# Kernel optimization log

Hardware: AMD Instinct MI355X
Metric: run time of the kernel (lower is better)

## Reference

```python
import jax, jax.numpy as jnp
import numpy as np

N = 100_000      # nodes
E = 1_600_000    # edges (avg degree 16)
D = 64           # input_dim
H = 64           # hidden_dim
G = 2048         # graphs in batch
EPS = 1e-5       # BatchNorm eps


def setup_inputs() -> dict:
    key = jax.random.key(0)
    ks = jax.random.split(key, 12)
    x = jax.random.normal(ks[0], (N, D), dtype=jnp.float32)
    edge_index = jax.random.randint(ks[1], (2, E), 0, N, dtype=jnp.int64)
    batch = jnp.sort(jax.random.randint(ks[2], (N,), 0, G, dtype=jnp.int64))
    s = 1.0 / np.sqrt(D)
    W1 = jax.random.normal(ks[3], (D, H), dtype=jnp.float32) * s
    b1 = jnp.zeros((H,), jnp.float32)
    g1 = jnp.ones((H,), jnp.float32)
    bt1 = jnp.zeros((H,), jnp.float32)
    W2 = jax.random.normal(ks[4], (H, H), dtype=jnp.float32) * s
    b2 = jnp.zeros((H,), jnp.float32)
    g2 = jnp.ones((H,), jnp.float32)
    bt2 = jnp.zeros((H,), jnp.float32)
    return {"x": x, "edge_index": edge_index, "batch": batch,
            "W1": W1, "b1": b1, "g1": g1, "bt1": bt1,
            "W2": W2, "b2": b2, "g2": g2, "bt2": bt2,
            "num_graphs": G}


def reference(x, edge_index, batch, W1, b1, g1, bt1, W2, b2, g2, bt2, num_graphs):
    n = x.shape[0]
    # GCN normalization with added self-loops (PyG GCNConv default)
    loops = jnp.arange(n, dtype=edge_index.dtype)
    src = jnp.concatenate([edge_index[0], loops])
    dst = jnp.concatenate([edge_index[1], loops])
    deg = jax.ops.segment_sum(jnp.ones(src.shape, jnp.float32), dst, num_segments=n)
    dis = jax.lax.rsqrt(jnp.maximum(deg, 1.0))  # deg >= 1 with self-loops
    norm = dis[src] * dis[dst]                  # [E+N]

    def gcn(h, W, b):
        h = h @ W                               # [N,H] dense transform first
        msg = h[src] * norm[:, None]            # gather + scale  [E+N, H]
        return jax.ops.segment_sum(msg, dst, num_segments=n) + b

    def bn(h, gamma, beta):
        mu = h.mean(axis=0)
        var = h.var(axis=0)
        return (h - mu) * jax.lax.rsqrt(var + EPS) * gamma + beta

    h = jax.nn.relu(bn(gcn(x, W1, b1), g1, bt1))
    h = jax.nn.relu(bn(gcn(h, W2, b2), g2, bt2))

    # global mean pool over graph ids
    ones = jnp.ones((n,), jnp.float32)
    counts = jax.ops.segment_sum(ones, batch, num_segments=num_graphs)
    sums = jax.ops.segment_sum(h, batch, num_segments=num_graphs)
    return sums / jnp.maximum(counts, 1.0)[:, None]
```

## Files before the change

kernel.cpp:

```cpp
#include <hip/hip_runtime.h>
#include <hip/hip_bf16.h>

#define BN_EPS 1e-5f
#define CCHUNK 8192

__device__ __forceinline__ float bf2f(ushort u) {
    return __uint_as_float(((unsigned int)u) << 16);
}
__device__ __forceinline__ ushort f2bf(float f) {
    unsigned int u = __float_as_uint(f);
    u += 0x7FFFu + ((u >> 16) & 1u);
    return (ushort)(u >> 16);
}

__global__ void k_bhist(const int* __restrict__ dst, int E, int nb, int* __restrict__ bktcnt) {
    __shared__ int lh[1024];
    for (int j = threadIdx.x; j < nb; j += 256) lh[j] = 0;
    __syncthreads();
    for (int i = blockIdx.x * blockDim.x + threadIdx.x; i < E; i += gridDim.x * blockDim.x)
        atomicAdd(&lh[dst[i] >> 7], 1);
    __syncthreads();
    for (int j = threadIdx.x; j < nb; j += 256) {
        int c = lh[j];
        if (c) atomicAdd(&bktcnt[j], c);
    }
}

__global__ void k_bscan(const int* __restrict__ bktcnt, int nb, int N,
                        int* __restrict__ bktoff, int* __restrict__ gpos,
                        int* __restrict__ rowptr) {
    __shared__ int sh[256];
    int tid = threadIdx.x;
    int base = tid * 4;
    int v[4]; int tsum = 0;
    #pragma unroll
    for (int k = 0; k < 4; ++k) {
        int i = base + k;
        v[k] = (i < nb) ? bktcnt[i] : 0;
        tsum += v[k];
    }
    sh[tid] = tsum;
    __syncthreads();
    for (int off = 1; off < 256; off <<= 1) {
        int add = (tid >= off) ? sh[tid - off] : 0;
        __syncthreads();
        sh[tid] += add;
        __syncthreads();
    }
    int excl = sh[tid] - tsum;
    #pragma unroll
    for (int k = 0; k < 4; ++k) {
        int i = base + k;
        if (i <= nb) {
            bktoff[i] = excl;
            if (i < nb) gpos[i] = excl;
        }
        excl += v[k];
    }
    if (tid == 255) rowptr[N] = sh[255];
}

__global__ void k_partition(const int* __restrict__ src, const int* __restrict__ dst,
                            int E, int nb, int sb,
                            int* __restrict__ gpos, unsigned int* __restrict__ eb) {
    __shared__ int lh[1024];
    int e0 = blockIdx.x * CCHUNK;
    int cnt = min(CCHUNK, E - e0);
    for (int j = threadIdx.x; j < nb; j += 256) lh[j] = 0;
    __syncthreads();
    for (int k = threadIdx.x; k < cnt; k += 256)
        atomicAdd(&lh[dst[e0 + k] >> 7], 1);
    __syncthreads();
    for (int j = threadIdx.x; j < nb; j += 256) {
        int c = lh[j];
        if (c) lh[j] = atomicAdd(&gpos[j], c);
    }
    __syncthreads();
    for (int k = threadIdx.x; k < cnt; k += 256) {
        int d = dst[e0 + k];
        unsigned int s = (unsigned int)src[e0 + k];
        int pos = atomicAdd(&lh[d >> 7], 1);
        eb[pos] = (((unsigned int)(d & 127)) << sb) | s;
    }
}

__global__ void k_row(const unsigned int* __restrict__ eb, const int* __restrict__ bktoff,
                      int sb, int N, float* __restrict__ dis, int* __restrict__ rowptr) {
    __shared__ int h[128];
    __shared__ int p[128];
    int tid = threadIdx.x;
    int b = blockIdx.x;
    if (tid < 128) h[tid] = 0;
    __syncthreads();
    int e0 = bktoff[b], e1 = bktoff[b + 1];
    for (int e = e0 + tid; e < e1; e += 256)
        atomicAdd(&h[(eb[e] >> sb) & 127], 1);
    __syncthreads();
    if (tid < 128) p[tid] = h[tid];
    __syncthreads();
    for (int off = 1; off < 128; off <<= 1) {
        int add = (tid < 128 && tid >= off) ? p[tid - off] : 0;
        __syncthreads();
        if (tid < 128) p[tid] += add;
        __syncthreads();
    }
    if (tid < 128) {
        int d = b * 128 + tid;
        if (d < N) {
            rowptr[d] = e0 + p[tid] - h[tid];
            dis[d] = rsqrtf((float)(h[tid] + 1));
        }
    }
}

__global__ void k_csrfill(const unsigned int* __restrict__ eb, const int* __restrict__ bktoff,
                          const int* __restrict__ rowptr, const float* __restrict__ dis,
                          int sb, unsigned int smask, int N,
                          int* __restrict__ cs, float* __restrict__ wf) {
    __shared__ int nc[128];
    __shared__ float dl[128];
    int tid = threadIdx.x;
    int b = blockIdx.x;
    if (tid < 128) {
        int d = b * 128 + tid;
        nc[tid] = (d < N) ? rowptr[d] : 0;
        dl[tid] = (d < N) ? dis[d] : 1.f;
    }
    __syncthreads();
    int e0 = bktoff[b], e1 = bktoff[b + 1];
    for (int e = e0 + tid; e < e1; e += 256) {
        unsigned int v = eb[e];
        int dloc = (v >> sb) & 127;
        int s = (int)(v & smask);
        int slot = atomicAdd(&nc[dloc], 1);
        cs[slot] = s;
        wf[slot] = dis[s] * dl[dloc];
    }
}

__global__ void k_matmul64t(const float* __restrict__ X, const float* __restrict__ W,
                            const float* __restrict__ bnp, int n, ushort* __restrict__ tb) {
    __shared__ float Xs[64][68];
    __shared__ float Ws[64][64];
    const int tid = threadIdx.x;
    const int rowbase = blockIdx.x * 64;

    {
        const float4* W4 = (const float4*)W;
        float4* Ws4 = (float4*)&Ws[0][0];
        #pragma unroll
        for (int k = 0; k < 4; ++k) Ws4[tid + 256 * k] = W4[tid + 256 * k];
    }
    {
        const int r  = tid >> 2;
        const int c0 = (tid & 3) * 16;
        const int row = rowbase + r;
        #pragma unroll
        for (int j = 0; j < 4; ++j) {
            float4 v;
            if (row < n) v = *(const float4*)&X[(size_t)row * 64 + c0 + 4 * j];
            else v = make_float4(0.f, 0.f, 0.f, 0.f);
            float vv[4] = {v.x, v.y, v.z, v.w};
            #pragma unroll
            for (int i = 0; i < 4; ++i) {
                int c = c0 + 4 * j + i;
                float f = vv[i];
                if (bnp) f = fmaxf(0.f, fmaf(f, bnp[c], bnp[64 + c]));
                Xs[c][r] = f;
            }
        }
    }
    __syncthreads();

    const int r0 = (tid & 15) * 4;
    const int c0 = (tid >> 4) * 4;
    float acc[4][4];
    #pragma unroll
    for (int i = 0; i < 4; ++i)
        #pragma unroll
        for (int j = 0; j < 4; ++j) acc[i][j] = 0.f;

    #pragma unroll 4
    for (int k = 0; k < 64; ++k) {
        float4 xv = *(const float4*)&Xs[k][r0];
        float4 wv = *(const float4*)&Ws[k][c0];
        float xa[4] = {xv.x, xv.y, xv.z, xv.w};
        float wa[4] = {wv.x, wv.y, wv.z, wv.w};
        #pragma unroll
        for (int i = 0; i < 4; ++i)
            #pragma unroll
            for (int j = 0; j < 4; ++j)
                acc[i][j] = fmaf(xa[i], wa[j], acc[i][j]);
    }

    #pragma unroll
    for (int i = 0; i < 4; ++i) {
        int row = rowbase + r0 + i;
        if (row < n) {
            ushort4 o;
            o.x = f2bf(acc[i][0]); o.y = f2bf(acc[i][1]);
            o.z = f2bf(acc[i][2]); o.w = f2bf(acc[i][3]);
            *(ushort4*)&tb[(size_t)row * 64 + c0] = o;
        }
    }
}

__global__ void k_gather(const int* __restrict__ cs, const float* __restrict__ wf,
                         const int* __restrict__ rowptr, const float* __restrict__ dis,
                         const ushort* __restrict__ tb, int n, float* __restrict__ a) {
    int lane = threadIdx.x & 63;
    int wave = threadIdx.x >> 6;
    int row = blockIdx.x * 4 + wave;
    if (row >= n) return;
    const int fl = lane & 7;
    const int o  = lane >> 3;
    int e0 = rowptr[row], e1 = rowptr[row + 1];
    float acc[8];
    #pragma unroll
    for (int i = 0; i < 8; ++i) acc[i] = 0.f;
    for (int base = e0; base < e1; base += 64) {
        int cnt = min(64, e1 - base);
        int   p  = (lane < cnt) ? cs[base + lane] : 0;
        float wv = (lane < cnt) ? wf[base + lane] : 0.f;
        int nq = (cnt + 7) >> 3;
        for (int j = 0; j < nq; ++j) {
            int idx = 8 * j + o;
            int s = __shfl(p, idx);
            float w = __shfl(wv, idx);
            uint4 tv = *(const uint4*)&tb[(size_t)s * 64 + 8 * fl];
            acc[0] = fmaf(__uint_as_float(tv.x << 16),         w, acc[0]);
            acc[1] = fmaf(__uint_as_float(tv.x & 0xffff0000u), w, acc[1]);
            acc[2] = fmaf(__uint_as_float(tv.y << 16),         w, acc[2]);
            acc[3] = fmaf(__uint_as_float(tv.y & 0xffff0000u), w, acc[3]);
            acc[4] = fmaf(__uint_as_float(tv.z << 16),         w, acc[4]);
            acc[5] = fmaf(__uint_as_float(tv.z & 0xffff0000u), w, acc[5]);
            acc[6] = fmaf(__uint_as_float(tv.w << 16),         w, acc[6]);
            acc[7] = fmaf(__uint_as_float(tv.w & 0xffff0000u), w, acc[7]);
        }
    }
    #pragma unroll
    for (int i = 0; i < 8; ++i) {
        acc[i] += __shfl_xor(acc[i], 8);
        acc[i] += __shfl_xor(acc[i], 16);
        acc[i] += __shfl_xor(acc[i], 32);
    }
    if (o == 0) {
        float dr = dis[row];
        float d2 = dr * dr;
        uint4 ts = *(const uint4*)&tb[(size_t)row * 64 + 8 * fl];
        acc[0] = fmaf(__uint_as_float(ts.x << 16),         d2, acc[0]);
        acc[1] = fmaf(__uint_as_float(ts.x & 0xffff0000u), d2, acc[1]);
        acc[2] = fmaf(__uint_as_float(ts.y << 16),         d2, acc[2]);
        acc[3] = fmaf(__uint_as_float(ts.y & 0xffff0000u), d2, acc[3]);
        acc[4] = fmaf(__uint_as_float(ts.z << 16),         d2, acc[4]);
        acc[5] = fmaf(__uint_as_float(ts.z & 0xffff0000u), d2, acc[5]);
        acc[6] = fmaf(__uint_as_float(ts.w << 16),         d2, acc[6]);
        acc[7] = fmaf(__uint_as_float(ts.w & 0xffff0000u), d2, acc[7]);
        float4 o0 = make_float4(acc[0], acc[1], acc[2], acc[3]);
        float4 o1 = make_float4(acc[4], acc[5], acc[6], acc[7]);
        *(float4*)&a[(size_t)row * 64 + 8 * fl]     = o0;
        *(float4*)&a[(size_t)row * 64 + 8 * fl + 4] = o1;
    }
}

__global__ void k_stats(const float* __restrict__ a, int n, float* __restrict__ stats) {
    int c = threadIdx.x & 63;
    int grp = threadIdx.x >> 6;
    float s = 0.f, s2 = 0.f;
    for (int r = blockIdx.x * 4 + grp; r < n; r += gridDim.x * 4) {
        float v = a[(size_t)r * 64 + c];
        s += v; s2 += v * v;
    }
    __shared__ float sh[2][4][64];
    sh[0][grp][c] = s; sh[1][grp][c] = s2;
    __syncthreads();
    if (threadIdx.x < 64) {
        float S  = sh[0][0][c] + sh[0][1][c] + sh[0][2][c] + sh[0][3][c];
        float S2 = sh[1][0][c] + sh[1][1][c] + sh[1][2][c] + sh[1][3][c];
        atomicAdd(&stats[c], S);
        atomicAdd(&stats[64 + c], S2);
    }
}

__global__ void k_bnparams(const float* __restrict__ stats, const float* __restrict__ g,
                           const float* __restrict__ bt, int n, float* __restrict__ bnp) {
    int c = threadIdx.x;
    if (c < 64) {
        float inv_n = 1.f / (float)n;
        float mean = stats[c] * inv_n;
        float var = stats[64 + c] * inv_n - mean * mean;
        float s = g[c] * rsqrtf(var + BN_EPS);
        bnp[c] = s;
        bnp[64 + c] = bt[c] - mean * s;
    }
}

__global__ void k_gbound(const int* __restrict__ batch, int n, int G, int* __restrict__ gs) {
    int g = blockIdx.x * blockDim.x + threadIdx.x;
    if (g > G) return;
    int lo = 0, hi = n;
    while (lo < hi) { int mid = (lo + hi) >> 1; if (batch[mid] < g) lo = mid + 1; else hi = mid; }
    gs[g] = lo;
}

__global__ void k_pool2(const float* __restrict__ a, const float* __restrict__ bnp,
                        const int* __restrict__ gs, int G, float* __restrict__ out) {
    int lane = threadIdx.x & 63;
    int wave = threadIdx.x >> 6;
    int g = blockIdx.x * 4 + wave;
    if (g >= G) return;
    int s = gs[g], e = gs[g + 1];
    float sc = bnp[lane], of = bnp[64 + lane];
    float acc = 0.f;
    for (int r = s; r < e; ++r)
        acc += fmaxf(0.f, fmaf(a[(size_t)r * 64 + lane], sc, of));
    out[(size_t)g * 64 + lane] = acc / (float)max(e - s, 1);
}

extern "C" void kernel_launch(void* const* d_in, const int* in_sizes, int n_in,
                              void* d_out, int out_size, void* d_ws, size_t ws_size,
                              hipStream_t stream) {
    const float* x     = (const float*)d_in[0];
    const int*   ei    = (const int*)d_in[1];
    const int*   batch = (const int*)d_in[2];
    const float* W1    = (const float*)d_in[3];
    const float* g1    = (const float*)d_in[5];
    const float* bt1   = (const float*)d_in[6];
    const float* W2    = (const float*)d_in[7];
    const float* g2    = (const float*)d_in[9];
    const float* bt2   = (const float*)d_in[10];

    const int N = in_sizes[0] / 64;
    const int E = in_sizes[1] / 2;
    const int G = out_size / 64;

    const int* src = ei;
    const int* dst = ei + E;

    const int nb = (N + 127) >> 7;
    int sb = 0; while ((1 << sb) < N) ++sb;
    const unsigned int smask = (1u << sb) - 1u;

    ushort* tb        = (ushort*)d_ws;
    float* a          = (float*)(tb + (size_t)N * 64);
    int*   cs         = (int*)(a + (size_t)N * 64);
    float* wf         = (float*)(cs + E);
    unsigned int* eb  = (unsigned int*)(wf + E);
    float* dis        = (float*)(eb + E);
    int*   rowptr     = (int*)(dis + N);
    int*   bktcnt     = rowptr + N + 1;
    float* stats      = (float*)(bktcnt + nb);
    int*   bktoff     = (int*)(stats + 256);
    int*   gpos       = bktoff + nb + 1;
    float* bnp        = (float*)(gpos + nb);
    int*   gs         = (int*)(bnp + 128);

    float* out = (float*)d_out;

    const int mmBlocks = (N + 63) / 64;
    const int gaBlocks = (N + 3) / 4;
    const int pcBlocks = (E + CCHUNK - 1) / CCHUNK;

    hipMemsetAsync(bktcnt, 0, (size_t)(nb + 256) * sizeof(int), stream);
    k_bhist<<<256, 256, 0, stream>>>(dst, E, nb, bktcnt);
    k_bscan<<<1, 256, 0, stream>>>(bktcnt, nb, N, bktoff, gpos, rowptr);
    k_partition<<<pcBlocks, 256, 0, stream>>>(src, dst, E, nb, sb, gpos, eb);
    k_row<<<nb, 256, 0, stream>>>(eb, bktoff, sb, N, dis, rowptr);
    k_csrfill<<<nb, 256, 0, stream>>>(eb, bktoff, rowptr, dis, sb, smask, N, cs, wf);
    k_gbound<<<(G + 256) / 256, 256, 0, stream>>>(batch, N, G, gs);

    k_matmul64t<<<mmBlocks, 256, 0, stream>>>(x, W1, nullptr, N, tb);
    k_gather<<<gaBlocks, 256, 0, stream>>>(cs, wf, rowptr, dis, tb, N, a);
    k_stats<<<512, 256, 0, stream>>>(a, N, stats);
    k_bnparams<<<1, 64, 0, stream>>>(stats, g1, bt1, N, bnp);

    k_matmul64t<<<mmBlocks, 256, 0, stream>>>(a, W2, bnp, N, tb);
    k_gather<<<gaBlocks, 256, 0, stream>>>(cs, wf, rowptr, dis, tb, N, a);
    k_stats<<<512, 256, 0, stream>>>(a, N, stats + 128);
    k_bnparams<<<1, 64, 0, stream>>>(stats + 128, g2, bt2, N, bnp);

    k_pool2<<<(G + 3) / 4, 256, 0, stream>>>(a, bnp, gs, G, out);
}
```

Before: 304.0 us.

## Fuse BN stats into gather, fold BN params into consumers, pack CSR

The column sum and sum-of-squares are now accumulated inside a persistent grid-stride gather kernel, which drops the separate stats pass over the activations. The BN scale and shift are computed per block inside the matmul and pool kernels instead of in separate tiny kernels. The graph-boundary search moves into the histogram kernel, and the column indices and weights are packed into one int2 array so each edge needs a single load. Launch count and memory traffic go down, at the cost of shared-memory atomics in the gather and fewer, longer-lived gather blocks that may balance load less evenly. CCHUNK is also doubled.

```diff
diff --git a/kernel.cpp b/kernel.cpp
--- a/kernel.cpp
+++ b/kernel.cpp
@@ -2,18 +2,22 @@
 #include <hip/hip_bf16.h>
 
 #define BN_EPS 1e-5f
-#define CCHUNK 8192
-
-__device__ __forceinline__ float bf2f(ushort u) {
-    return __uint_as_float(((unsigned int)u) << 16);
-}
+#define CCHUNK 16384
+
 __device__ __forceinline__ ushort f2bf(float f) {
     unsigned int u = __float_as_uint(f);
     u += 0x7FFFu + ((u >> 16) & 1u);
     return (ushort)(u >> 16);
 }
 
-__global__ void k_bhist(const int* __restrict__ dst, int E, int nb, int* __restrict__ bktcnt) {
+__global__ void k_bhist(const int* __restrict__ dst, int E, int nb, int* __restrict__ bktcnt,
+                        const int* __restrict__ batch, int n, int G, int* __restrict__ gs) {
+    int gid = blockIdx.x * blockDim.x + threadIdx.x;
+    if (gid <= G) {
+        int lo = 0, hi = n;
+        while (lo < hi) { int mid = (lo + hi) >> 1; if (batch[mid] < gid) lo = mid + 1; else hi = mid; }
+        gs[gid] = lo;
+    }
     __shared__ int lh[1024];
     for (int j = threadIdx.x; j < nb; j += 256) lh[j] = 0;
     __syncthreads();
@@ -115,8 +119,7 @@
 
 __global__ void k_csrfill(const unsigned int* __restrict__ eb, const int* __restrict__ bktoff,
                           const int* __restrict__ rowptr, const float* __restrict__ dis,
-                          int sb, unsigned int smask, int N,
-                          int* __restrict__ cs, float* __restrict__ wf) {
+                          int sb, unsigned int smask, int N, int2* __restrict__ cw) {
     __shared__ int nc[128];
     __shared__ float dl[128];
     int tid = threadIdx.x;
@@ -133,23 +136,36 @@
         int dloc = (v >> sb) & 127;
         int s = (int)(v & smask);
         int slot = atomicAdd(&nc[dloc], 1);
-        cs[slot] = s;
-        wf[slot] = dis[s] * dl[dloc];
+        cw[slot] = make_int2(s, __float_as_int(dis[s] * dl[dloc]));
     }
 }
 
 __global__ void k_matmul64t(const float* __restrict__ X, const float* __restrict__ W,
-                            const float* __restrict__ bnp, int n, ushort* __restrict__ tb) {
+                            const float* __restrict__ stats, const float* __restrict__ gamma,
+                            const float* __restrict__ beta, int n, ushort* __restrict__ tb) {
     __shared__ float Xs[64][68];
     __shared__ float Ws[64][64];
+    __shared__ float bnpL[128];
     const int tid = threadIdx.x;
     const int rowbase = blockIdx.x * 64;
+    const bool hasbn = (stats != nullptr);
 
     {
         const float4* W4 = (const float4*)W;
         float4* Ws4 = (float4*)&Ws[0][0];
         #pragma unroll
         for (int k = 0; k < 4; ++k) Ws4[tid + 256 * k] = W4[tid + 256 * k];
+    }
+    if (hasbn) {
+        if (tid < 64) {
+            float inv_n = 1.f / (float)n;
+            float mean = stats[tid] * inv_n;
+            float var = stats[64 + tid] * inv_n - mean * mean;
+            float s = gamma[tid] * rsqrtf(var + BN_EPS);
+            bnpL[tid] = s;
+            bnpL[64 + tid] = beta[tid] - mean * s;
+        }
+        __syncthreads();
     }
     {
         const int r  = tid >> 2;
@@ -165,7 +181,7 @@
             for (int i = 0; i < 4; ++i) {
                 int c = c0 + 4 * j + i;
                 float f = vv[i];
-                if (bnp) f = fmaxf(0.f, fmaf(f, bnp[c], bnp[64 + c]));
+                if (hasbn) f = fmaxf(0.f, fmaf(f, bnpL[c], bnpL[64 + c]));
                 Xs[c][r] = f;
             }
         }
@@ -205,112 +221,103 @@
     }
 }
 
-__global__ void k_gather(const int* __restrict__ cs, const float* __restrict__ wf,
-                         const int* __restrict__ rowptr, const float* __restrict__ dis,
-                         const ushort* __restrict__ tb, int n, float* __restrict__ a) {
-    int lane = threadIdx.x & 63;
-    int wave = threadIdx.x >> 6;
-    int row = blockIdx.x * 4 + wave;
-    if (row >= n) return;
+__global__ void k_gather(const int2* __restrict__ cw, const int* __restrict__ rowptr,
+                         const float* __restrict__ dis, const ushort* __restrict__ tb,
+                         int n, float* __restrict__ a, float* __restrict__ stats) {
+    __shared__ float ls[128];
+    int tid = threadIdx.x;
+    if (tid < 128) ls[tid] = 0.f;
+    __syncthreads();
+    int lane = tid & 63;
+    int wave = tid >> 6;
     const int fl = lane & 7;
     const int o  = lane >> 3;
-    int e0 = rowptr[row], e1 = rowptr[row + 1];
-    float acc[8];
-    #pragma unroll
-    for (int i = 0; i < 8; ++i) acc[i] = 0.f;
-    for (int base = e0; base < e1; base += 64) {
-        int cnt = min(64, e1 - base);
-        int   p  = (lane < cnt) ? cs[base + lane] : 0;
-        float wv = (lane < cnt) ? wf[base + lane] : 0.f;
-        int nq = (cnt + 7) >> 3;
-        for (int j = 0; j < nq; ++j) {
-            int idx = 8 * j + o;
-            int s = __shfl(p, idx);
-            float w = __shfl(wv, idx);
-            uint4 tv = *(const uint4*)&tb[(size_t)s * 64 + 8 * fl];
-            acc[0] = fmaf(__uint_as_float(tv.x << 16),         w, acc[0]);
-            acc[1] = fmaf(__uint_as_float(tv.x & 0xffff0000u), w, acc[1]);
-            acc[2] = fmaf(__uint_as_float(tv.y << 16),         w, acc[2]);
-            acc[3] = fmaf(__uint_as_float(tv.y & 0xffff0000u), w, acc[3]);
-            acc[4] = fmaf(__uint_as_float(tv.z << 16),         w, acc[4]);
-            acc[5] = fmaf(__uint_as_float(tv.z & 0xffff0000u), w, acc[5]);
-            acc[6] = fmaf(__uint_as_float(tv.w << 16),         w, acc[6]);
-            acc[7] = fmaf(__uint_as_float(tv.w & 0xffff0000u), w, acc[7]);
-        }
-    }
-    #pragma unroll
-    for (int i = 0; i < 8; ++i) {
-        acc[i] += __shfl_xor(acc[i], 8);
-        acc[i] += __shfl_xor(acc[i], 16);
-        acc[i] += __shfl_xor(acc[i], 32);
+    float psum[8], psq[8];
+    #pragma unroll
+    for (int i = 0; i < 8; ++i) { psum[i] = 0.f; psq[i] = 0.f; }
+
+    for (int row = blockIdx.x * 4 + wave; row < n; row += gridDim.x * 4) {
+        int e0 = rowptr[row], e1 = rowptr[row + 1];
+        float acc[8];
+        #pragma unroll
+        for (int i = 0; i < 8; ++i) acc[i] = 0.f;
+        for (int base = e0; base < e1; base += 64) {
+            int cnt = min(64, e1 - base);
+            int2 pw = (lane < cnt) ? cw[base + lane] : make_int2(0, 0);
+            int nq = (cnt + 7) >> 3;
+            for (int j = 0; j < nq; ++j) {
+                int idx = 8 * j + o;
+                int s = __shfl(pw.x, idx);
+                float w = __uint_as_float((unsigned int)__shfl(pw.y, idx));
+                uint4 tv = *(const uint4*)&tb[(size_t)s * 64 + 8 * fl];
+                acc[0] = fmaf(__uint_as_float(tv.x << 16),         w, acc[0]);
+                acc[1] = fmaf(__uint_as_float(tv.x & 0xffff0000u), w, acc[1]);
+                acc[2] = fmaf(__uint_as_float(tv.y << 16),         w, acc[2]);
+                acc[3] = fmaf(__uint_as_float(tv.y & 0xffff0000u), w, acc[3]);
+                acc[4] = fmaf(__uint_as_float(tv.z << 16),         w, acc[4]);
+                acc[5] = fmaf(__uint_as_float(tv.z & 0xffff0000u), w, acc[5]);
+                acc[6] = fmaf(__uint_as_float(tv.w << 16),         w, acc[6]);
+                acc[7] = fmaf(__uint_as_float(tv.w & 0xffff0000u), w, acc[7]);
+            }
+        }
+        #pragma unroll
+        for (int i = 0; i < 8; ++i) {
+            acc[i] += __shfl_xor(acc[i], 8);
+            acc[i] += __shfl_xor(acc[i], 16);
+            acc[i] += __shfl_xor(acc[i], 32);
+        }
+        if (o == 0) {
+            float dr = dis[row];
+            float d2 = dr * dr;
+            uint4 ts = *(const uint4*)&tb[(size_t)row * 64 + 8 * fl];
+            acc[0] = fmaf(__uint_as_float(ts.x << 16),         d2, acc[0]);
+            acc[1] = fmaf(__uint_as_float(ts.x & 0xffff0000u), d2, acc[1]);
+            acc[2] = fmaf(__uint_as_float(ts.y << 16),         d2, acc[2]);
+            acc[3] = fmaf(__uint_as_float(ts.y & 0xffff0000u), d2, acc[3]);
+            acc[4] = fmaf(__uint_as_float(ts.z << 16),         d2, acc[4]);
+            acc[5] = fmaf(__uint_as_float(ts.z & 0xffff0000u), d2, acc[5]);
+            acc[6] = fmaf(__uint_as_float(ts.w << 16),         d2, acc[6]);
+            acc[7] = fmaf(__uint_as_float(ts.w & 0xffff0000u), d2, acc[7]);
+            *(float4*)&a[(size_t)row * 64 + 8 * fl]     = make_float4(acc[0], acc[1], acc[2], acc[3]);
+            *(float4*)&a[(size_t)row * 64 + 8 * fl + 4] = make_float4(acc[4], acc[5], acc[6], acc[7]);
+            #pragma unroll
+            for (int i = 0; i < 8; ++i) {
+                psum[i] += acc[i];
+                psq[i] = fmaf(acc[i], acc[i], psq[i]);
+            }
+        }
     }
     if (o == 0) {
-        float dr = dis[row];
-        float d2 = dr * dr;
-        uint4 ts = *(const uint4*)&tb[(size_t)row * 64 + 8 * fl];
-        acc[0] = fmaf(__uint_as_float(ts.x << 16),         d2, acc[0]);
-        acc[1] = fmaf(__uint_as_float(ts.x & 0xffff0000u), d2, acc[1]);
-        acc[2] = fmaf(__uint_as_float(ts.y << 16),         d2, acc[2]);
-        acc[3] = fmaf(__uint_as_float(ts.y & 0xffff0000u), d2, acc[3]);
-        acc[4] = fmaf(__uint_as_float(ts.z << 16),         d2, acc[4]);
-        acc[5] = fmaf(__uint_as_float(ts.z & 0xffff0000u), d2, acc[5]);
-        acc[6] = fmaf(__uint_as_float(ts.w << 16),         d2, acc[6]);
-        acc[7] = fmaf(__uint_as_float(ts.w & 0xffff0000u), d2, acc[7]);
-        float4 o0 = make_float4(acc[0], acc[1], acc[2], acc[3]);
-        float4 o1 = make_float4(acc[4], acc[5], acc[6], acc[7]);
-        *(float4*)&a[(size_t)row * 64 + 8 * fl]     = o0;
-        *(float4*)&a[(size_t)row * 64 + 8 * fl + 4] = o1;
-    }
-}
-
-__global__ void k_stats(const float* __restrict__ a, int n, float* __restrict__ stats) {
-    int c = threadIdx.x & 63;
-    int grp = threadIdx.x >> 6;
-    float s = 0.f, s2 = 0.f;
-    for (int r = blockIdx.x * 4 + grp; r < n; r += gridDim.x * 4) {
-        float v = a[(size_t)r * 64 + c];
-        s += v; s2 += v * v;
-    }
-    __shared__ float sh[2][4][64];
-    sh[0][grp][c] = s; sh[1][grp][c] = s2;
-    __syncthreads();
-    if (threadIdx.x < 64) {
-        float S  = sh[0][0][c] + sh[0][1][c] + sh[0][2][c] + sh[0][3][c];
-        float S2 = sh[1][0][c] + sh[1][1][c] + sh[1][2][c] + sh[1][3][c];
-        atomicAdd(&stats[c], S);
-        atomicAdd(&stats[64 + c], S2);
-    }
-}
-
-__global__ void k_bnparams(const float* __restrict__ stats, const float* __restrict__ g,
-                           const float* __restrict__ bt, int n, float* __restrict__ bnp) {
-    int c = threadIdx.x;
-    if (c < 64) {
+        #pragma unroll
+        for (int i = 0; i < 8; ++i) {
+            atomicAdd(&ls[8 * fl + i], psum[i]);
+            atomicAdd(&ls[64 + 8 * fl + i], psq[i]);
+        }
+    }
+    __syncthreads();
+    if (tid < 128) atomicAdd(&stats[tid], ls[tid]);
+}
+
+__global__ void k_pool2(const float* __restrict__ a, const float* __restrict__ stats,
+                        const float* __restrict__ gamma, const float* __restrict__ beta,
+                        const int* __restrict__ gs, int n, int G, float* __restrict__ out) {
+    __shared__ float bnpL[128];
+    int tid = threadIdx.x;
+    if (tid < 64) {
         float inv_n = 1.f / (float)n;
-        float mean = stats[c] * inv_n;
-        float var = stats[64 + c] * inv_n - mean * mean;
-        float s = g[c] * rsqrtf(var + BN_EPS);
-        bnp[c] = s;
-        bnp[64 + c] = bt[c] - mean * s;
-    }
-}
-
-__global__ void k_gbound(const int* __restrict__ batch, int n, int G, int* __restrict__ gs) {
-    int g = blockIdx.x * blockDim.x + threadIdx.x;
-    if (g > G) return;
-    int lo = 0, hi = n;
-    while (lo < hi) { int mid = (lo + hi) >> 1; if (batch[mid] < g) lo = mid + 1; else hi = mid; }
-    gs[g] = lo;
-}
-
-__global__ void k_pool2(const float* __restrict__ a, const float* __restrict__ bnp,
-                        const int* __restrict__ gs, int G, float* __restrict__ out) {
-    int lane = threadIdx.x & 63;
-    int wave = threadIdx.x >> 6;
+        float mean = stats[tid] * inv_n;
+        float var = stats[64 + tid] * inv_n - mean * mean;
+        float s = gamma[tid] * rsqrtf(var + BN_EPS);
+        bnpL[tid] = s;
+        bnpL[64 + tid] = beta[tid] - mean * s;
+    }
+    __syncthreads();
+    int lane = tid & 63;
+    int wave = tid >> 6;
     int g = blockIdx.x * 4 + wave;
     if (g >= G) return;
     int s = gs[g], e = gs[g + 1];
-    float sc = bnp[lane], of = bnp[64 + lane];
+    float sc = bnpL[lane], of = bnpL[64 + lane];
     float acc = 0.f;
     for (int r = s; r < e; ++r)
         acc += fmaxf(0.f, fmaf(a[(size_t)r * 64 + lane], sc, of));
@@ -343,41 +350,34 @@
 
     ushort* tb        = (ushort*)d_ws;
     float* a          = (float*)(tb + (size_t)N * 64);
-    int*   cs         = (int*)(a + (size_t)N * 64);
-    float* wf         = (float*)(cs + E);
-    unsigned int* eb  = (unsigned int*)(wf + E);
+    int2*  cw         = (int2*)(a + (size_t)N * 64);
+    unsigned int* eb  = (unsigned int*)(cw + E);
     float* dis        = (float*)(eb + E);
     int*   rowptr     = (int*)(dis + N);
     int*   bktcnt     = rowptr + N + 1;
     float* stats      = (float*)(bktcnt + nb);
     int*   bktoff     = (int*)(stats + 256);
     int*   gpos       = bktoff + nb + 1;
-    float* bnp        = (float*)(gpos + nb);
-    int*   gs         = (int*)(bnp + 128);
+    int*   gs         = gpos + nb;
 
     float* out = (float*)d_out;
 
     const int mmBlocks = (N + 63) / 64;
-    const int gaBlocks = (N + 3) / 4;
+    const int gaBlocks = 2048;
     const int pcBlocks = (E + CCHUNK - 1) / CCHUNK;
 
     hipMemsetAsync(bktcnt, 0, (size_t)(nb + 256) * sizeof(int), stream);
-    k_bhist<<<256, 256, 0, stream>>>(dst, E, nb, bktcnt);
+    k_bhist<<<256, 256, 0, stream>>>(dst, E, nb, bktcnt, batch, N, G, gs);
     k_bscan<<<1, 256, 0, stream>>>(bktcnt, nb, N, bktoff, gpos, rowptr);
     k_partition<<<pcBlocks, 256, 0, stream>>>(src, dst, E, nb, sb, gpos, eb);
     k_row<<<nb, 256, 0, stream>>>(eb, bktoff, sb, N, dis, rowptr);
-    k_csrfill<<<nb, 256, 0, stream>>>(eb, bktoff, rowptr, dis, sb, smask, N, cs, wf);
-    k_gbound<<<(G + 256) / 256, 256, 0, stream>>>(batch, N, G, gs);
-
-    k_matmul64t<<<mmBlocks, 256, 0, stream>>>(x, W1, nullptr, N, tb);
-    k_gather<<<gaBlocks, 256, 0, stream>>>(cs, wf, rowptr, dis, tb, N, a);
-    k_stats<<<512, 256, 0, stream>>>(a, N, stats);
-    k_bnparams<<<1, 64, 0, stream>>>(stats, g1, bt1, N, bnp);
-
-    k_matmul64t<<<mmBlocks, 256, 0, stream>>>(a, W2, bnp, N, tb);
-    k_gather<<<gaBlocks, 256, 0, stream>>>(cs, wf, rowptr, dis, tb, N, a);
-    k_stats<<<512, 256, 0, stream>>>(a, N, stats + 128);
-    k_bnparams<<<1, 64, 0, stream>>>(stats + 128, g2, bt2, N, bnp);
-
-    k_pool2<<<(G + 3) / 4, 256, 0, stream>>>(a, bnp, gs, G, out);
-}
+    k_csrfill<<<nb, 256, 0, stream>>>(eb, bktoff, rowptr, dis, sb, smask, N, cw);
+
+    k_matmul64t<<<mmBlocks, 256, 0, stream>>>(x, W1, nullptr, nullptr, nullptr, N, tb);
+    k_gather<<<gaBlocks, 256, 0, stream>>>(cw, rowptr, dis, tb, N, a, stats);
+
+    k_matmul64t<<<mmBlocks, 256, 0, stream>>>(a, W2, stats, g1, bt1, N, tb);
+    k_gather<<<gaBlocks, 256, 0, stream>>>(cw, rowptr, dis, tb, N, a, stats + 128);
+
+    k_pool2<<<(G + 3) / 4, 256, 0, stream>>>(a, stats + 128, g2, bt2, gs, N, G, out);
+}
```

Measured after the change: 352.5 us. +15.9%, slower.
